# Kernel optimization log

Measured on AMD Instinct MI355X. Metric: run time of the kernel, lower is better.

Reference implementation:

```python
import jax, jax.numpy as jnp
import numpy as np

D = 1024  # d_model (all ATTENTION_CONST widths)
N = 4096  # sequence length


def setup_inputs() -> dict:
    key = jax.random.key(0)
    ks = jax.random.split(key, 11)
    s = 1.0 / np.sqrt(D)
    return {
        "q": jax.random.normal(ks[0], (N, D), jnp.float32),
        "k": jax.random.normal(ks[1], (N, D), jnp.float32),
        "v": jax.random.normal(ks[2], (N, D), jnp.float32),
        "wq_w": jax.random.normal(ks[3], (D, D), jnp.float32) * s,
        "wq_b": jax.random.normal(ks[4], (D,), jnp.float32) * s,
        "wk_w": jax.random.normal(ks[5], (D, D), jnp.float32) * s,
        "wk_b": jax.random.normal(ks[6], (D,), jnp.float32) * s,
        "wv_w": jax.random.normal(ks[7], (D, D), jnp.float32) * s,
        "wv_b": jax.random.normal(ks[8], (D,), jnp.float32) * s,
        "wo_w": jax.random.normal(ks[9], (D, D), jnp.float32) * s,
        "wo_b": jax.random.normal(ks[10], (D,), jnp.float32) * s,
    }


def reference(q, k, v, wq_w, wq_b, wk_w, wk_b, wv_w, wv_b, wo_w, wo_b):
    # Linear projections (torch convention: y = x @ W.T + b)
    qp = q @ wq_w.T + wq_b  # [N, D]
    kp = k @ wk_w.T + wk_b  # [N, D]
    vp = v @ wv_w.T + wv_b  # [N, D]
    # Naive attention: NO sqrt(d) scaling, NO head split (faithful to source)
    scores = qp @ kp.T                      # [N, N]
    attention_weights = jax.nn.softmax(scores, axis=-1)
    x = attention_weights @ vp              # [N, D]
    x = x @ wo_w.T + wo_b                   # output projection
    return (x, attention_weights)
```

## Files before the change

### kernel.cpp

```cpp
#include <hip/hip_runtime.h>
#include <cstdint>

#define N_SEQ 4096
#define DMODEL 1024

#define BM 128
#define BN 128
#define BN2 64
#define UNITE 4096

typedef __bf16 bf16_t;
typedef _Float16 f16_t;
typedef f16_t f16x8 __attribute__((ext_vector_type(8)));
typedef f16_t f16x4 __attribute__((ext_vector_type(4)));
typedef float f32x4 __attribute__((ext_vector_type(4)));

typedef __attribute__((address_space(1))) void* as1ptr;
typedef __attribute__((address_space(3))) void* as3ptr;

__device__ __forceinline__ void gload16(const void* g, void* l) {
  __builtin_amdgcn_global_load_lds((as1ptr)(uintptr_t)g, (as3ptr)(uintptr_t)l,
                                   16, 0, 0);
}

#define SBAR() asm volatile("s_barrier" ::: "memory")
#define WAITLGKM(n)                                              \
  do {                                                           \
    asm volatile("s_waitcnt lgkmcnt(" #n ")" ::: "memory");      \
    __builtin_amdgcn_sched_barrier(0);                           \
  } while (0)
#define WAITVM(n) asm volatile("s_waitcnt vmcnt(" #n ")" ::: "memory")

__global__ __launch_bounds__(256)
void qkv_proj(const f16_t* __restrict__ qh, const f16_t* __restrict__ ql,
              const f16_t* __restrict__ wq, const float* __restrict__ wq_b,
              const f16_t* __restrict__ kh, const f16_t* __restrict__ kl,
              const f16_t* __restrict__ wk, const float* __restrict__ wk_b,
              const f16_t* __restrict__ vh, const f16_t* __restrict__ wv,
              const float* __restrict__ wv_b,
              f16_t* __restrict__ QPh, f16_t* __restrict__ KPh,
              f16_t* __restrict__ VPt)
{
  __shared__ __align__(16) f16_t lds[6 * UNITE];

  const int z = blockIdx.z;
  const f16_t *A0, *A1 = nullptr, *B0;
  const float* bias;
  if (z == 0)      { A0 = qh; A1 = ql; B0 = wq; bias = wq_b; }
  else if (z == 1) { A0 = kh; A1 = kl; B0 = wk; bias = wk_b; }
  else             { A0 = vh;          B0 = wv; bias = wv_b; }
  const bool twop = (z < 2);

  const int M = N_SEQ, Nc = DMODEL, K = DMODEL;
  const int t = threadIdx.x;
  const int lane = t & 63;
  const int wave = t >> 6;
  const int wm = wave >> 1;
  const int wn = wave & 1;

  const int gx = gridDim.x;
  const int nwg = gx * gridDim.y;
  const int flat = blockIdx.y * gx + blockIdx.x;
  const int swz = (flat & 7) * (nwg >> 3) + (flat >> 3);
  const int row0 = (swz / gx) * BM;
  const int col0 = (swz % gx) * BN;

  const int srw = t >> 3;
  const int scol = 8 * ((t & 7) ^ ((t >> 3) & 7));
  const int sdst = t * 8;

  const int fr = lane & 15;
  const int kq = (lane >> 4) * 8;
  const int sw = (fr & 7) << 3;

  f32x4 acc[4][4] = {};

  for (int k0 = 0; k0 < K; k0 += 64) {
#pragma unroll
    for (int h = 0; h < 2; ++h) {
      const int r = h * 32 + srw;
      gload16(A0 + (size_t)(row0 + r) * K + k0 + scol,
              &lds[0 * UNITE + h * 2048 + sdst]);
      gload16(A0 + (size_t)(row0 + 64 + r) * K + k0 + scol,
              &lds[1 * UNITE + h * 2048 + sdst]);
      gload16(B0 + (size_t)(col0 + r) * K + k0 + scol,
              &lds[4 * UNITE + h * 2048 + sdst]);
      gload16(B0 + (size_t)(col0 + 64 + r) * K + k0 + scol,
              &lds[5 * UNITE + h * 2048 + sdst]);
      if (twop) {
        gload16(A1 + (size_t)(row0 + r) * K + k0 + scol,
                &lds[2 * UNITE + h * 2048 + sdst]);
        gload16(A1 + (size_t)(row0 + 64 + r) * K + k0 + scol,
                &lds[3 * UNITE + h * 2048 + sdst]);
      }
    }
    __syncthreads();

    f16x8 ah[4][2], al[4][2], bh[4][2];
#pragma unroll
    for (int m = 0; m < 4; ++m) {
      const int r = (m * 16 + fr) * 64;
#pragma unroll
      for (int ks = 0; ks < 2; ++ks) {
        const int c = (ks * 32 + kq) ^ sw;
        ah[m][ks] = *(const f16x8*)&lds[wm * UNITE + r + c];
        if (twop) al[m][ks] = *(const f16x8*)&lds[(2 + wm) * UNITE + r + c];
      }
    }
#pragma unroll
    for (int n = 0; n < 4; ++n) {
      const int r = (n * 16 + fr) * 64;
#pragma unroll
      for (int ks = 0; ks < 2; ++ks)
        bh[n][ks] = *(const f16x8*)&lds[(4 + wn) * UNITE + r +
                                        (((ks * 32 + kq)) ^ sw)];
    }

#pragma unroll
    for (int m = 0; m < 4; ++m)
#pragma unroll
      for (int n = 0; n < 4; ++n)
#pragma unroll
        for (int ks = 0; ks < 2; ++ks) {
          acc[m][n] = __builtin_amdgcn_mfma_f32_16x16x32_f16(
              ah[m][ks], bh[n][ks], acc[m][n], 0, 0, 0);
          if (twop)
            acc[m][n] = __builtin_amdgcn_mfma_f32_16x16x32_f16(
                al[m][ks], bh[n][ks], acc[m][n], 0, 0, 0);
        }
    __syncthreads();
  }

#pragma unroll
  for (int m = 0; m < 4; ++m) {
#pragma unroll
    for (int n = 0; n < 4; ++n) {
      const int grow0 = row0 + wm * 64 + m * 16 + (lane >> 4) * 4;
      const int gcol = col0 + wn * 64 + n * 16 + (lane & 15);
      const float bv = bias[gcol];
      if (z == 2) {
        f16x4 p;
#pragma unroll
        for (int r = 0; r < 4; ++r) p[r] = (f16_t)(acc[m][n][r] + bv);
        *(f16x4*)&VPt[(size_t)gcol * M + grow0] = p;
      } else {
        f16_t* out = (z == 0) ? QPh : KPh;
#pragma unroll
        for (int r = 0; r < 4; ++r)
          out[(size_t)(grow0 + r) * Nc + gcol] = (f16_t)(acc[m][n][r] + bv);
      }
    }
  }
}

template <int OUT_F32>
__global__ __launch_bounds__(256)
void gemm_f16p(const f16_t* __restrict__ A, const f16_t* __restrict__ B,
               const float* __restrict__ bias,
               f16_t* __restrict__ Cf16, float* __restrict__ Cf32,
               int M, int Nc, int K)
{
  __shared__ __align__(16) f16_t lds[2 * 3 * UNITE];

  const int gx = gridDim.x;
  const int nwg = gx * gridDim.y;
  const int flat = blockIdx.y * gx + blockIdx.x;
  const int swz = (flat & 7) * (nwg >> 3) + (flat >> 3);
  const int bx = swz % gx;
  const int by = swz / gx;

  const int t = threadIdx.x;
  const int lane = t & 63;
  const int wave = t >> 6;
  const int wm = wave >> 1;
  const int wn = wave & 1;
  const int row0 = by * BM;
  const int col0 = bx * BN2;

  const int srw = t >> 3;
  const int scol = 8 * ((t & 7) ^ ((t >> 3) & 7));
  const int sdst = t * 8;

  const int fr = lane & 15;
  const int kq = (lane >> 4) * 8;
  const int sw = (fr & 7) << 3;

  auto stage = [&](int buf, int kt) {
    const int k0 = kt << 6;
#pragma unroll
    for (int h = 0; h < 2; ++h) {
      const int r = h * 32 + srw;
      gload16(A + (size_t)(row0 + r) * K + k0 + scol,
              &lds[(buf * 3 + 0) * UNITE + h * 2048 + sdst]);
      gload16(A + (size_t)(row0 + 64 + r) * K + k0 + scol,
              &lds[(buf * 3 + 1) * UNITE + h * 2048 + sdst]);
      gload16(B + (size_t)(col0 + r) * K + k0 + scol,
              &lds[(buf * 3 + 2) * UNITE + h * 2048 + sdst]);
    }
  };

  f32x4 acc[4][2] = {};
  const int NT = K >> 6;

  stage(0, 0);
  stage(1, 1);
  WAITVM(6);
  SBAR();

  for (int kt = 0; kt < NT; ++kt) {
    const int p = kt & 1;
    const f16_t* Ab = &lds[(p * 3 + wm) * UNITE];
    const f16_t* Bb = &lds[(p * 3 + 2) * UNITE];

    f16x8 ah[4][2], bh[2][2];
#pragma unroll
    for (int m = 0; m < 2; ++m)
#pragma unroll
      for (int ks = 0; ks < 2; ++ks)
        ah[m][ks] = *(const f16x8*)&Ab[(m * 16 + fr) * 64 +
                                       ((ks * 32 + kq) ^ sw)];
#pragma unroll
    for (int n = 0; n < 2; ++n)
#pragma unroll
      for (int ks = 0; ks < 2; ++ks)
        bh[n][ks] = *(const f16x8*)&Bb[(wn * 32 + n * 16 + fr) * 64 +
                                       ((ks * 32 + kq) ^ sw)];
#pragma unroll
    for (int m = 2; m < 4; ++m)
#pragma unroll
      for (int ks = 0; ks < 2; ++ks)
        ah[m][ks] = *(const f16x8*)&Ab[(m * 16 + fr) * 64 +
                                       ((ks * 32 + kq) ^ sw)];

    WAITLGKM(4);
#pragma unroll
    for (int m = 0; m < 2; ++m)
#pragma unroll
      for (int n = 0; n < 2; ++n)
#pragma unroll
        for (int ks = 0; ks < 2; ++ks)
          acc[m][n] = __builtin_amdgcn_mfma_f32_16x16x32_f16(
              ah[m][ks], bh[n][ks], acc[m][n], 0, 0, 0);
    WAITLGKM(0);
#pragma unroll
    for (int m = 2; m < 4; ++m)
#pragma unroll
      for (int n = 0; n < 2; ++n)
#pragma unroll
        for (int ks = 0; ks < 2; ++ks)
          acc[m][n] = __builtin_amdgcn_mfma_f32_16x16x32_f16(
              ah[m][ks], bh[n][ks], acc[m][n], 0, 0, 0);

    SBAR();
    if (kt + 2 < NT) {
      stage(p, kt + 2);
      WAITVM(6);
    } else if (kt + 1 < NT) {
      WAITVM(0);
    }
    SBAR();
  }

#pragma unroll
  for (int m = 0; m < 4; ++m) {
#pragma unroll
    for (int n = 0; n < 2; ++n) {
      const int grow0 = row0 + wm * 64 + m * 16 + (lane >> 4) * 4;
      const int gcol = col0 + wn * 32 + n * 16 + (lane & 15);
#pragma unroll
      for (int r = 0; r < 4; ++r) {
        const size_t idx = (size_t)(grow0 + r) * Nc + gcol;
        if (OUT_F32) Cf32[idx] = acc[m][n][r] + bias[gcol];
        else         Cf16[idx] = (f16_t)acc[m][n][r];
      }
    }
  }
}

__global__ __launch_bounds__(256)
void gemm_f16s(const f16_t* __restrict__ A, const f16_t* __restrict__ B,
               float* __restrict__ C, int M, int Nc, int K)
{
  __shared__ __align__(16) f16_t lds[2 * 4 * UNITE];

  const int gx = gridDim.x;
  const int nwg = gx * gridDim.y;
  const int flat = blockIdx.y * gx + blockIdx.x;
  const int swz = (flat & 7) * (nwg >> 3) + (flat >> 3);
  const int bx = swz % gx;
  const int by = swz / gx;

  const int t = threadIdx.x;
  const int lane = t & 63;
  const int wave = t >> 6;
  const int wm = wave >> 1;
  const int wn = wave & 1;
  const int row0 = by * BM;
  const int col0 = bx * BN;

  const int srw = t >> 3;
  const int scol = 8 * ((t & 7) ^ ((t >> 3) & 7));
  const int sdst = t * 8;

  const int fr = lane & 15;
  const int kq = (lane >> 4) * 8;
  const int sw = (fr & 7) << 3;

  auto stage = [&](int buf, int kt) {
    const int k0 = kt << 6;
#pragma unroll
    for (int h = 0; h < 2; ++h) {
      const int r = h * 32 + srw;
      gload16(A + (size_t)(row0 + r) * K + k0 + scol,
              &lds[(buf * 4 + 0) * UNITE + h * 2048 + sdst]);
      gload16(A + (size_t)(row0 + 64 + r) * K + k0 + scol,
              &lds[(buf * 4 + 1) * UNITE + h * 2048 + sdst]);
      gload16(B + (size_t)(col0 + r) * K + k0 + scol,
              &lds[(buf * 4 + 2) * UNITE + h * 2048 + sdst]);
      gload16(B + (size_t)(col0 + 64 + r) * K + k0 + scol,
              &lds[(buf * 4 + 3) * UNITE + h * 2048 + sdst]);
    }
  };

  f32x4 acc[4][4] = {};
  const int NT = K >> 6;

  stage(0, 0);
  stage(1, 1);
  WAITVM(8);
  SBAR();

  for (int kt = 0; kt < NT; ++kt) {
    const int p = kt & 1;
    const f16_t* Ab = &lds[(p * 4 + wm) * UNITE];
    const f16_t* Bb = &lds[(p * 4 + 2 + wn) * UNITE];

    f16x8 ah[4][2], bh[4][2];
#pragma unroll
    for (int m = 0; m < 4; ++m)
#pragma unroll
      for (int ks = 0; ks < 2; ++ks)
        ah[m][ks] = *(const f16x8*)&Ab[(m * 16 + fr) * 64 +
                                       ((ks * 32 + kq) ^ sw)];
#pragma unroll
    for (int n = 0; n < 2; ++n)
#pragma unroll
      for (int ks = 0; ks < 2; ++ks)
        bh[n][ks] = *(const f16x8*)&Bb[(n * 16 + fr) * 64 +
                                       ((ks * 32 + kq) ^ sw)];
#pragma unroll
    for (int n = 2; n < 4; ++n)
#pragma unroll
      for (int ks = 0; ks < 2; ++ks)
        bh[n][ks] = *(const f16x8*)&Bb[(n * 16 + fr) * 64 +
                                       ((ks * 32 + kq) ^ sw)];

    WAITLGKM(4);
#pragma unroll
    for (int m = 0; m < 4; ++m)
#pragma unroll
      for (int n = 0; n < 2; ++n)
#pragma unroll
        for (int ks = 0; ks < 2; ++ks)
          acc[m][n] = __builtin_amdgcn_mfma_f32_16x16x32_f16(
              ah[m][ks], bh[n][ks], acc[m][n], 0, 0, 0);
    WAITLGKM(0);
#pragma unroll
    for (int m = 0; m < 4; ++m)
#pragma unroll
      for (int n = 2; n < 4; ++n)
#pragma unroll
        for (int ks = 0; ks < 2; ++ks)
          acc[m][n] = __builtin_amdgcn_mfma_f32_16x16x32_f16(
              ah[m][ks], bh[n][ks], acc[m][n], 0, 0, 0);

    SBAR();
    if (kt + 2 < NT) {
      stage(p, kt + 2);
      WAITVM(8);
    } else if (kt + 1 < NT) {
      WAITVM(0);
    }
    SBAR();
  }

#pragma unroll
  for (int m = 0; m < 4; ++m) {
#pragma unroll
    for (int n = 0; n < 4; ++n) {
      const int grow0 = row0 + wm * 64 + m * 16 + (lane >> 4) * 4;
      const int gcol = col0 + wn * 64 + n * 16 + (lane & 15);
#pragma unroll
      for (int r = 0; r < 4; ++r)
        C[(size_t)(grow0 + r) * Nc + gcol] = acc[m][n][r];
    }
  }
}

struct SplitDesc {
  const float* src[7];
  f16_t* hi[7];
  f16_t* lo[7];
  int mode[7];
  int blk_start[8];
};

__global__ __launch_bounds__(256)
void split_all(SplitDesc d)
{
  const int b = blockIdx.x;
  int seg = 0;
#pragma unroll
  for (int s = 1; s < 7; ++s) seg += (b >= d.blk_start[s]) ? 1 : 0;
  const int i = (b - d.blk_start[seg]) * 256 + threadIdx.x;
  const float4 v = ((const float4*)d.src[seg])[i];
  const float vv[4] = {v.x, v.y, v.z, v.w};
  f16x4 h, l;
#pragma unroll
  for (int j = 0; j < 4; ++j) {
    const f16_t hh = (f16_t)vv[j];
    h[j] = hh;
    l[j] = (f16_t)(vv[j] - (float)hh);
  }
  ((f16x4*)d.hi[seg])[i] = h;
  if (d.mode[seg] == 2) ((f16x4*)d.lo[seg])[i] = l;
}

__global__ __launch_bounds__(256)
void softmax_rows(float* __restrict__ S, f16_t* __restrict__ P, int n)
{
  const int row = blockIdx.x;
  float* srow = S + (size_t)row * n;
  f16_t* prow = P + (size_t)row * n;
  const int t = threadIdx.x;
  const int lane = t & 63;
  const int wave = t >> 6;
  __shared__ float red[8];

  float4 v[4];
  float mx = -3.4e38f;
#pragma unroll
  for (int i = 0; i < 4; ++i) {
    v[i] = *(const float4*)(srow + (size_t)(i * 256 + t) * 4);
    mx = fmaxf(mx, fmaxf(fmaxf(v[i].x, v[i].y), fmaxf(v[i].z, v[i].w)));
  }
#pragma unroll
  for (int off = 32; off > 0; off >>= 1) mx = fmaxf(mx, __shfl_xor(mx, off));
  if (lane == 0) red[wave] = mx;
  __syncthreads();
  mx = fmaxf(fmaxf(red[0], red[1]), fmaxf(red[2], red[3]));

  float e[16];
  float sum = 0.f;
#pragma unroll
  for (int i = 0; i < 4; ++i) {
    e[4 * i + 0] = __expf(v[i].x - mx);
    e[4 * i + 1] = __expf(v[i].y - mx);
    e[4 * i + 2] = __expf(v[i].z - mx);
    e[4 * i + 3] = __expf(v[i].w - mx);
    sum += e[4 * i + 0] + e[4 * i + 1] + e[4 * i + 2] + e[4 * i + 3];
  }
#pragma unroll
  for (int off = 32; off > 0; off >>= 1) sum += __shfl_xor(sum, off);
  if (lane == 0) red[4 + wave] = sum;
  __syncthreads();
  sum = red[4] + red[5] + red[6] + red[7];
  const float inv = 1.0f / sum;

#pragma unroll
  for (int i = 0; i < 4; ++i) {
    float4 w;
    w.x = e[4 * i + 0] * inv;
    w.y = e[4 * i + 1] * inv;
    w.z = e[4 * i + 2] * inv;
    w.w = e[4 * i + 3] * inv;
    *(float4*)(srow + (size_t)(i * 256 + t) * 4) = w;
    f16x4 p;
    p[0] = (f16_t)w.x;
    p[1] = (f16_t)w.y;
    p[2] = (f16_t)w.z;
    p[3] = (f16_t)w.w;
    *(f16x4*)(prow + (size_t)(i * 256 + t) * 4) = p;
  }
}

extern "C" void kernel_launch(void* const* d_in, const int* in_sizes, int n_in,
                              void* d_out, int out_size, void* d_ws, size_t ws_size,
                              hipStream_t stream) {
  const int N = N_SEQ, D = DMODEL;
  const float* q    = (const float*)d_in[0];
  const float* k    = (const float*)d_in[1];
  const float* v    = (const float*)d_in[2];
  const float* wq_w = (const float*)d_in[3];
  const float* wq_b = (const float*)d_in[4];
  const float* wk_w = (const float*)d_in[5];
  const float* wk_b = (const float*)d_in[6];
  const float* wv_w = (const float*)d_in[7];
  const float* wv_b = (const float*)d_in[8];
  const float* wo_w = (const float*)d_in[9];
  const float* wo_b = (const float*)d_in[10];

  float* x_out = (float*)d_out;
  float* attn  = x_out + (size_t)N * D;

  char* wsp = (char*)d_ws;
  auto alloc = [&](size_t bytes) { char* p = wsp; wsp += bytes; return p; };
  const size_t ND = (size_t)N * D, DD = (size_t)D * D;
  f16_t*  qh16  = (f16_t*)alloc(ND * 2);
  f16_t*  ql16  = (f16_t*)alloc(ND * 2);
  f16_t*  kh16  = (f16_t*)alloc(ND * 2);
  f16_t*  kl16  = (f16_t*)alloc(ND * 2);
  f16_t*  vh16  = (f16_t*)alloc(ND * 2);
  f16_t*  wq16  = (f16_t*)alloc(DD * 2);
  f16_t*  wk16  = (f16_t*)alloc(DD * 2);
  f16_t*  wv16  = (f16_t*)alloc(DD * 2);
  f16_t*  wo16  = (f16_t*)alloc(DD * 2);
  f16_t*  QPh   = (f16_t*)alloc(ND * 2);
  f16_t*  pad1  = (f16_t*)alloc(ND * 2);
  f16_t*  KPh   = (f16_t*)alloc(ND * 2);
  f16_t*  pad2  = (f16_t*)alloc(ND * 2);
  f16_t*  VPt   = (f16_t*)alloc(ND * 2);
  f16_t*  Pb    = QPh;
  f16_t*  Xb    = vh16;
  (void)pad1; (void)pad2;

  SplitDesc sd;
  sd.src[0] = q;    sd.hi[0] = qh16;  sd.lo[0] = ql16;    sd.mode[0] = 2;
  sd.src[1] = k;    sd.hi[1] = kh16;  sd.lo[1] = kl16;    sd.mode[1] = 2;
  sd.src[2] = v;    sd.hi[2] = vh16;  sd.lo[2] = nullptr; sd.mode[2] = 3;
  sd.src[3] = wq_w; sd.hi[3] = wq16;  sd.lo[3] = nullptr; sd.mode[3] = 3;
  sd.src[4] = wk_w; sd.hi[4] = wk16;  sd.lo[4] = nullptr; sd.mode[4] = 3;
  sd.src[5] = wv_w; sd.hi[5] = wv16;  sd.lo[5] = nullptr; sd.mode[5] = 3;
  sd.src[6] = wo_w; sd.hi[6] = wo16;  sd.lo[6] = nullptr; sd.mode[6] = 3;
  const int nb_nd = (int)(ND / 4 / 256);
  const int nb_dd = (int)(DD / 4 / 256);
  sd.blk_start[0] = 0;
  sd.blk_start[1] = nb_nd;
  sd.blk_start[2] = 2 * nb_nd;
  sd.blk_start[3] = 3 * nb_nd;
  sd.blk_start[4] = 3 * nb_nd + nb_dd;
  sd.blk_start[5] = 3 * nb_nd + 2 * nb_dd;
  sd.blk_start[6] = 3 * nb_nd + 3 * nb_dd;
  sd.blk_start[7] = 3 * nb_nd + 4 * nb_dd;
  split_all<<<dim3(sd.blk_start[7]), dim3(256), 0, stream>>>(sd);

  const dim3 blk(256);
  const dim3 gsc(N / BN, N / BM);
  const dim3 gd(D / BN2, N / BM);

  qkv_proj<<<dim3(D / BN, N / BM, 3), blk, 0, stream>>>(
      qh16, ql16, wq16, wq_b,
      kh16, kl16, wk16, wk_b,
      vh16, wv16, wv_b,
      QPh, KPh, VPt);

  gemm_f16s<<<gsc, blk, 0, stream>>>(QPh, KPh, attn, N, N, D);

  softmax_rows<<<dim3(N), blk, 0, stream>>>(attn, Pb, N);

  gemm_f16p<0><<<gd, blk, 0, stream>>>(
      Pb, VPt, nullptr, Xb, nullptr, N, D, N);

  gemm_f16p<1><<<gd, blk, 0, stream>>>(
      Xb, wo16, wo_b, nullptr, x_out, N, D, D);
}
```

Before: 196.2 us.

## Double-buffer QKV projection K-loop and flatten hi/lo passes into one stream

Restructures the QKV projection GEMM so the hi and lo A operands are processed as consecutive K tiles (32 iterations for Q/K, 16 for V) instead of two MFMAs per tile. It adds a two-stage LDS double buffer with global_load_lds prefetch two tiles ahead and manual vmcnt/lgkmcnt waits, splitting B fragment reads so the first half of the MFMAs can start before all LDS reads finish. The aim is to hide global load latency behind compute. In exchange it uses more LDS per block, which may lower occupancy, and relies on hand-placed barriers and wait counts.

```diff
diff --git a/kernel.cpp b/kernel.cpp
--- a/kernel.cpp
+++ b/kernel.cpp
@@ -41,15 +41,15 @@
               f16_t* __restrict__ QPh, f16_t* __restrict__ KPh,
               f16_t* __restrict__ VPt)
 {
-  __shared__ __align__(16) f16_t lds[6 * UNITE];
+  __shared__ __align__(16) f16_t lds[2 * 4 * UNITE];
 
   const int z = blockIdx.z;
   const f16_t *A0, *A1 = nullptr, *B0;
   const float* bias;
   if (z == 0)      { A0 = qh; A1 = ql; B0 = wq; bias = wq_b; }
   else if (z == 1) { A0 = kh; A1 = kl; B0 = wk; bias = wk_b; }
-  else             { A0 = vh;          B0 = wv; bias = wv_b; }
-  const bool twop = (z < 2);
+  else             { A0 = vh; A1 = vh; B0 = wv; bias = wv_b; }
+  const int NT = (z < 2) ? 32 : 16;
 
   const int M = N_SEQ, Nc = DMODEL, K = DMODEL;
   const int t = threadIdx.x;
@@ -73,62 +73,82 @@
   const int kq = (lane >> 4) * 8;
   const int sw = (fr & 7) << 3;
 
-  f32x4 acc[4][4] = {};
-
-  for (int k0 = 0; k0 < K; k0 += 64) {
+  auto stage = [&](int buf, int kt) {
+    const f16_t* A = (kt >= 16) ? A1 : A0;
+    const int k0 = (kt & 15) << 6;
 #pragma unroll
     for (int h = 0; h < 2; ++h) {
       const int r = h * 32 + srw;
-      gload16(A0 + (size_t)(row0 + r) * K + k0 + scol,
-              &lds[0 * UNITE + h * 2048 + sdst]);
-      gload16(A0 + (size_t)(row0 + 64 + r) * K + k0 + scol,
-              &lds[1 * UNITE + h * 2048 + sdst]);
+      gload16(A + (size_t)(row0 + r) * K + k0 + scol,
+              &lds[(buf * 4 + 0) * UNITE + h * 2048 + sdst]);
+      gload16(A + (size_t)(row0 + 64 + r) * K + k0 + scol,
+              &lds[(buf * 4 + 1) * UNITE + h * 2048 + sdst]);
       gload16(B0 + (size_t)(col0 + r) * K + k0 + scol,
-              &lds[4 * UNITE + h * 2048 + sdst]);
+              &lds[(buf * 4 + 2) * UNITE + h * 2048 + sdst]);
       gload16(B0 + (size_t)(col0 + 64 + r) * K + k0 + scol,
-              &lds[5 * UNITE + h * 2048 + sdst]);
-      if (twop) {
-        gload16(A1 + (size_t)(row0 + r) * K + k0 + scol,
-                &lds[2 * UNITE + h * 2048 + sdst]);
-        gload16(A1 + (size_t)(row0 + 64 + r) * K + k0 + scol,
-                &lds[3 * UNITE + h * 2048 + sdst]);
-      }
-    }
-    __syncthreads();
-
-    f16x8 ah[4][2], al[4][2], bh[4][2];
-#pragma unroll
-    for (int m = 0; m < 4; ++m) {
-      const int r = (m * 16 + fr) * 64;
-#pragma unroll
-      for (int ks = 0; ks < 2; ++ks) {
-        const int c = (ks * 32 + kq) ^ sw;
-        ah[m][ks] = *(const f16x8*)&lds[wm * UNITE + r + c];
-        if (twop) al[m][ks] = *(const f16x8*)&lds[(2 + wm) * UNITE + r + c];
-      }
-    }
-#pragma unroll
-    for (int n = 0; n < 4; ++n) {
-      const int r = (n * 16 + fr) * 64;
-#pragma unroll
-      for (int ks = 0; ks < 2; ++ks)
-        bh[n][ks] = *(const f16x8*)&lds[(4 + wn) * UNITE + r +
-                                        (((ks * 32 + kq)) ^ sw)];
-    }
-
+              &lds[(buf * 4 + 3) * UNITE + h * 2048 + sdst]);
+    }
+  };
+
+  f32x4 acc[4][4] = {};
+
+  stage(0, 0);
+  stage(1, 1);
+  WAITVM(8);
+  SBAR();
+
+  for (int kt = 0; kt < NT; ++kt) {
+    const int p = kt & 1;
+    const f16_t* Ab = &lds[(p * 4 + wm) * UNITE];
+    const f16_t* Bb = &lds[(p * 4 + 2 + wn) * UNITE];
+
+    f16x8 ah[4][2], bh[4][2];
 #pragma unroll
     for (int m = 0; m < 4; ++m)
 #pragma unroll
-      for (int n = 0; n < 4; ++n)
-#pragma unroll
-        for (int ks = 0; ks < 2; ++ks) {
+      for (int ks = 0; ks < 2; ++ks)
+        ah[m][ks] = *(const f16x8*)&Ab[(m * 16 + fr) * 64 +
+                                       ((ks * 32 + kq) ^ sw)];
+#pragma unroll
+    for (int n = 0; n < 2; ++n)
+#pragma unroll
+      for (int ks = 0; ks < 2; ++ks)
+        bh[n][ks] = *(const f16x8*)&Bb[(n * 16 + fr) * 64 +
+                                       ((ks * 32 + kq) ^ sw)];
+#pragma unroll
+    for (int n = 2; n < 4; ++n)
+#pragma unroll
+      for (int ks = 0; ks < 2; ++ks)
+        bh[n][ks] = *(const f16x8*)&Bb[(n * 16 + fr) * 64 +
+                                       ((ks * 32 + kq) ^ sw)];
+
+    WAITLGKM(4);
+#pragma unroll
+    for (int m = 0; m < 4; ++m)
+#pragma unroll
+      for (int n = 0; n < 2; ++n)
+#pragma unroll
+        for (int ks = 0; ks < 2; ++ks)
           acc[m][n] = __builtin_amdgcn_mfma_f32_16x16x32_f16(
               ah[m][ks], bh[n][ks], acc[m][n], 0, 0, 0);
-          if (twop)
-            acc[m][n] = __builtin_amdgcn_mfma_f32_16x16x32_f16(
-                al[m][ks], bh[n][ks], acc[m][n], 0, 0, 0);
-        }
-    __syncthreads();
+    WAITLGKM(0);
+#pragma unroll
+    for (int m = 0; m < 4; ++m)
+#pragma unroll
+      for (int n = 2; n < 4; ++n)
+#pragma unroll
+        for (int ks = 0; ks < 2; ++ks)
+          acc[m][n] = __builtin_amdgcn_mfma_f32_16x16x32_f16(
+              ah[m][ks], bh[n][ks], acc[m][n], 0, 0, 0);
+
+    SBAR();
+    if (kt + 2 < NT) {
+      stage(p, kt + 2);
+      WAITVM(8);
+    } else if (kt + 1 < NT) {
+      WAITVM(0);
+    }
+    SBAR();
   }
 
 #pragma unroll
```

After: 200.3 us. 2.1% more time.
